# Performance work log

Measured on AMD Instinct MI355X. Metric: run time of the kernel, lower is better.

## Reference

```python
import jax, jax.numpy as jnp
import numpy as np

VOCAB, D, PATCH, ROUNDS = 256, 64, 4, 3
B, T = 32, 8192


def setup_inputs() -> dict:
    key = jax.random.key(0)
    ks = jax.random.split(key, 16)
    s = 0.02
    inp = {
        "x": jax.random.randint(ks[0], (B, T), 0, VOCAB),
        "emb": jax.random.normal(ks[1], (VOCAB, D), jnp.float32) * s,
        # msg_net: Linear(2d->d), GELU, Linear(d->d); weights stored [in, out]
        "w_m1": jax.random.normal(ks[2], (2 * D, D), jnp.float32) * s,
        "b_m1": jnp.zeros((D,), jnp.float32),
        "w_m2": jax.random.normal(ks[3], (D, D), jnp.float32) * s,
        "b_m2": jnp.zeros((D,), jnp.float32),
        # update_net: Linear(2d->d), GELU, Linear(d->d)
        "w_u1": jax.random.normal(ks[4], (2 * D, D), jnp.float32) * s,
        "b_u1": jnp.zeros((D,), jnp.float32),
        "w_u2": jax.random.normal(ks[5], (D, D), jnp.float32) * s,
        "b_u2": jnp.zeros((D,), jnp.float32),
        # LayerNorm(d)
        "ln_g": jnp.ones((D,), jnp.float32),
        "ln_b": jnp.zeros((D,), jnp.float32),
        # readout: Linear(d -> vocab)
        "w_r": jax.random.normal(ks[6], (D, VOCAB), jnp.float32) * s,
        "b_r": jnp.zeros((VOCAB,), jnp.float32),
    }
    return inp


def _mlp(z, w1, b1, w2, b2):
    h = jax.nn.gelu(z @ w1 + b1, approximate=False)  # torch nn.GELU default = exact erf
    return h @ w2 + b2


def _layernorm(h, g, b, eps=1e-5):
    mu = jnp.mean(h, axis=-1, keepdims=True)
    var = jnp.mean((h - mu) ** 2, axis=-1, keepdims=True)
    return (h - mu) / jnp.sqrt(var + eps) * g + b


def reference(x, emb, w_m1, b_m1, w_m2, b_m2, w_u1, b_u1, w_u2, b_u2, ln_g, ln_b, w_r, b_r):
    Bx, Tx = x.shape
    P = PATCH
    N = (Tx + P - 1) // P
    xp = jnp.pad(x, ((0, 0), (0, N * P - Tx)))  # pad token id 0
    h = emb[xp].reshape(Bx, N, P, D).mean(axis=2)  # [B, N, d] patch-node features
    for _ in range(ROUNDS):
        left = jnp.pad(h[:, :-1], ((0, 0), (1, 0), (0, 0)))  # shift-right along N
        msgs = _mlp(jnp.concatenate([h, left], axis=-1), w_m1, b_m1, w_m2, b_m2)
        upd = _mlp(jnp.concatenate([h, msgs], axis=-1), w_u1, b_u1, w_u2, b_u2)
        h = _layernorm(h + upd, ln_g, ln_b)
    tok = jnp.repeat(h, P, axis=1)[:, :Tx]  # broadcast node feat to its P tokens
    return tok @ w_r + b_r  # [B, T, vocab]
```

## Files before the change

kernel.cpp:

```cpp
#include <hip/hip_runtime.h>
#include <hip/hip_bf16.h>
#include <math.h>

#define DD 64
#define NPB 2048
#define RTOT 65536

typedef __bf16 bf16;
typedef bf16 bf16x8 __attribute__((ext_vector_type(8)));
typedef float f32x4 __attribute__((ext_vector_type(4)));
typedef short short4v __attribute__((ext_vector_type(4)));

#define COMPILER_FENCE() asm volatile("" ::: "memory")

__device__ __forceinline__ f32x4 mfma16(bf16x8 a, bf16x8 b, f32x4 c) {
  return __builtin_amdgcn_mfma_f32_16x16x32_bf16(a, b, c, 0, 0, 0);
}

__device__ __forceinline__ float gelu_fast(float x) {
  float u = fabsf(x) * 0.70710678118654752f;
  float t = __builtin_amdgcn_rcpf(fmaf(0.3275911f, u, 1.0f));
  float p = t * fmaf(t, fmaf(t, fmaf(t, fmaf(t, 1.061405429f, -1.453152027f),
                                     1.421413741f), -0.284496736f), 0.254829592f);
  float e = __expf(-u * u);
  float erfa = fmaf(-p, e, 1.0f);
  float s = copysignf(erfa, x);
  return 0.5f * x * (1.0f + s);
}

__device__ __forceinline__ int swz(int col, int row) {
  return col ^ ((row & 7) << 3);
}

__device__ __forceinline__ bf16x8 ld8(const bf16* p) {
  return *reinterpret_cast<const bf16x8*>(p);
}

__global__ void __launch_bounds__(256) k_pe(const int* __restrict__ x,
                                            const float* __restrict__ emb,
                                            const float* __restrict__ wm1,
                                            const float* __restrict__ wm2,
                                            const float* __restrict__ wu1,
                                            const float* __restrict__ wu2,
                                            const float* __restrict__ wr,
                                            bf16* __restrict__ Wsc,
                                            bf16* __restrict__ h) {
  const int b = blockIdx.x;
  if (b < 160) {
    int gid = b * 256 + threadIdx.x;
    if (gid < 8192) {
      int n = gid >> 7, k = gid & 127;
      Wsc[gid] = (bf16)wm1[k * 64 + n];
    } else if (gid < 16384) {
      int j = gid - 8192, n = j >> 7, k = j & 127;
      Wsc[gid] = (bf16)wu1[k * 64 + n];
    } else if (gid < 20480) {
      int j = gid - 16384, n = j >> 6, k = j & 63;
      Wsc[gid] = (bf16)wm2[k * 64 + n];
    } else if (gid < 24576) {
      int j = gid - 20480, n = j >> 6, k = j & 63;
      Wsc[gid] = (bf16)wu2[k * 64 + n];
    } else {
      int j = gid - 24576, v = j >> 6, k = j & 63;
      Wsc[gid] = (bf16)wr[k * 256 + v];
    }
  } else {
    int gid = (b - 160) * 256 + threadIdx.x;
    int row = gid >> 4, d0 = (gid & 15) * 4;
    const int* xp = x + row * 4;
    f32x4 s = {0.f, 0.f, 0.f, 0.f};
#pragma unroll
    for (int p = 0; p < 4; ++p)
      s += *reinterpret_cast<const f32x4*>(emb + xp[p] * DD + d0);
    short4v o;
#pragma unroll
    for (int j = 0; j < 4; ++j)
      o[j] = (short)__builtin_bit_cast(unsigned short, (bf16)(s[j] * 0.25f));
    *reinterpret_cast<short4v*>(h + row * DD + d0) = o;
  }
}

__global__ void __launch_bounds__(256) k_r(const bf16* __restrict__ hin,
                                           bf16* __restrict__ hout,
                                           const bf16* __restrict__ Wsc,
                                           const float* __restrict__ bm1,
                                           const float* __restrict__ bm2,
                                           const float* __restrict__ bu1,
                                           const float* __restrict__ bu2,
                                           const float* __restrict__ lng,
                                           const float* __restrict__ lnb) {
  __shared__ bf16 W1[2][64 * 128];
  __shared__ bf16 Ms[64 * 64];
  __shared__ bf16 Hs[64 * 64];

  const int tid = threadIdx.x;
  const int lane = tid & 63;
  const int wv = tid >> 6;
  const int l15 = lane & 15;
  const int lhi = lane >> 4;

  for (int i = tid; i < 2048; i += 256) {
    int buf = i >> 10, idx = i & 1023;
    int n = idx >> 4, g = (idx & 15) * 8;
    *reinterpret_cast<bf16x8*>(&W1[buf][n * 128 + swz(g, n)]) =
        ld8(Wsc + buf * 8192 + n * 128 + g);
  }
  bf16x8 fm2[4][2], fu2[4][2];
#pragma unroll
  for (int ct = 0; ct < 4; ++ct)
#pragma unroll
    for (int kt = 0; kt < 2; ++kt) {
      int off = (ct * 16 + l15) * 64 + kt * 32 + lhi * 8;
      fm2[ct][kt] = ld8(Wsc + 16384 + off);
      fu2[ct][kt] = ld8(Wsc + 20480 + off);
    }
  float bm1v[4], bm2v[4], bu1v[4], bu2v[4], lngv[4], lnbv[4];
#pragma unroll
  for (int ct = 0; ct < 4; ++ct) {
    int c = ct * 16 + l15;
    bm1v[ct] = bm1[c]; bm2v[ct] = bm2[c];
    bu1v[ct] = bu1[c]; bu2v[ct] = bu2[c];
    lngv[ct] = lng[c]; lnbv[ct] = lnb[c];
  }
  __syncthreads();

  const int lrow = wv * 16 + l15;
  const int sxr = (lrow & 7) << 3;
  const int sxw = (l15 & 7) << 3;
  const f32x4 fz = {0.f, 0.f, 0.f, 0.f};

  for (int tt = 0; tt < 2; ++tt) {
    const int rowbase = (blockIdx.x * 2 + tt) * 64;
    const int grow = rowbase + lrow;
    const bf16* hrow = hin + (size_t)grow * DD;

    bf16x8 ah0 = ld8(hrow + lhi * 8);
    bf16x8 ah1 = ld8(hrow + 32 + lhi * 8);
    bf16x8 al0, al1;
#pragma unroll
    for (int j = 0; j < 8; ++j) { al0[j] = (bf16)0.f; al1[j] = (bf16)0.f; }
    if ((grow & (NPB - 1)) != 0) {
      al0 = ld8(hrow - DD + lhi * 8);
      al1 = ld8(hrow - DD + 32 + lhi * 8);
    }

    f32x4 acc[4];
#pragma unroll
    for (int ct = 0; ct < 4; ++ct) acc[ct] = fz;
#pragma unroll
    for (int ct = 0; ct < 4; ++ct) {
      const bf16* wb = &W1[0][(ct * 16 + l15) * 128];
      acc[ct] = mfma16(ah0, ld8(wb + ((lhi * 8) ^ sxw)), acc[ct]);
      acc[ct] = mfma16(ah1, ld8(wb + ((32 + lhi * 8) ^ sxw)), acc[ct]);
      acc[ct] = mfma16(al0, ld8(wb + ((64 + lhi * 8) ^ sxw)), acc[ct]);
      acc[ct] = mfma16(al1, ld8(wb + ((96 + lhi * 8) ^ sxw)), acc[ct]);
    }
#pragma unroll
    for (int ct = 0; ct < 4; ++ct)
#pragma unroll
      for (int r = 0; r < 4; ++r) {
        float g = gelu_fast(acc[ct][r] + bm1v[ct]);
        int row = wv * 16 + lhi * 4 + r;
        Hs[row * 64 + swz(ct * 16 + l15, row)] = (bf16)g;
      }
    COMPILER_FENCE();
#pragma unroll
    for (int ct = 0; ct < 4; ++ct) acc[ct] = fz;
    {
      bf16x8 g0 = ld8(&Hs[lrow * 64 + ((lhi * 8) ^ sxr)]);
      bf16x8 g1 = ld8(&Hs[lrow * 64 + ((32 + lhi * 8) ^ sxr)]);
#pragma unroll
      for (int ct = 0; ct < 4; ++ct) {
        acc[ct] = mfma16(g0, fm2[ct][0], acc[ct]);
        acc[ct] = mfma16(g1, fm2[ct][1], acc[ct]);
      }
    }
#pragma unroll
    for (int ct = 0; ct < 4; ++ct)
#pragma unroll
      for (int r = 0; r < 4; ++r) {
        int row = wv * 16 + lhi * 4 + r;
        Ms[row * 64 + swz(ct * 16 + l15, row)] = (bf16)(acc[ct][r] + bm2v[ct]);
      }
    COMPILER_FENCE();
#pragma unroll
    for (int ct = 0; ct < 4; ++ct) acc[ct] = fz;
    {
      bf16x8 m0 = ld8(&Ms[lrow * 64 + ((lhi * 8) ^ sxr)]);
      bf16x8 m1 = ld8(&Ms[lrow * 64 + ((32 + lhi * 8) ^ sxr)]);
#pragma unroll
      for (int ct = 0; ct < 4; ++ct) {
        const bf16* wb = &W1[1][(ct * 16 + l15) * 128];
        acc[ct] = mfma16(ah0, ld8(wb + ((lhi * 8) ^ sxw)), acc[ct]);
        acc[ct] = mfma16(ah1, ld8(wb + ((32 + lhi * 8) ^ sxw)), acc[ct]);
        acc[ct] = mfma16(m0, ld8(wb + ((64 + lhi * 8) ^ sxw)), acc[ct]);
        acc[ct] = mfma16(m1, ld8(wb + ((96 + lhi * 8) ^ sxw)), acc[ct]);
      }
    }
    COMPILER_FENCE();
#pragma unroll
    for (int ct = 0; ct < 4; ++ct)
#pragma unroll
      for (int r = 0; r < 4; ++r) {
        float g = gelu_fast(acc[ct][r] + bu1v[ct]);
        int row = wv * 16 + lhi * 4 + r;
        Hs[row * 64 + swz(ct * 16 + l15, row)] = (bf16)g;
      }
    COMPILER_FENCE();
#pragma unroll
    for (int ct = 0; ct < 4; ++ct) acc[ct] = fz;
    {
      bf16x8 u0 = ld8(&Hs[lrow * 64 + ((lhi * 8) ^ sxr)]);
      bf16x8 u1 = ld8(&Hs[lrow * 64 + ((32 + lhi * 8) ^ sxr)]);
#pragma unroll
      for (int ct = 0; ct < 4; ++ct) {
        acc[ct] = mfma16(u0, fu2[ct][0], acc[ct]);
        acc[ct] = mfma16(u1, fu2[ct][1], acc[ct]);
      }
    }
    float xv[4][4];
#pragma unroll
    for (int ct = 0; ct < 4; ++ct)
#pragma unroll
      for (int r = 0; r < 4; ++r) {
        int row = rowbase + wv * 16 + lhi * 4 + r;
        xv[ct][r] = acc[ct][r] + bu2v[ct] + (float)hin[(size_t)row * DD + ct * 16 + l15];
      }
    float s1[4], s2[4];
#pragma unroll
    for (int r = 0; r < 4; ++r) {
      s1[r] = 0.f; s2[r] = 0.f;
#pragma unroll
      for (int ct = 0; ct < 4; ++ct) { s1[r] += xv[ct][r]; s2[r] += xv[ct][r] * xv[ct][r]; }
    }
#pragma unroll
    for (int off = 1; off < 16; off <<= 1)
#pragma unroll
      for (int r = 0; r < 4; ++r) {
        s1[r] += __shfl_xor(s1[r], off);
        s2[r] += __shfl_xor(s2[r], off);
      }
#pragma unroll
    for (int r = 0; r < 4; ++r) {
      float mu = s1[r] * 0.015625f;
      float var = s2[r] * 0.015625f - mu * mu;
      float rstd = rsqrtf(var + 1e-5f);
      int row = rowbase + wv * 16 + lhi * 4 + r;
#pragma unroll
      for (int ct = 0; ct < 4; ++ct)
        hout[(size_t)row * DD + ct * 16 + l15] =
            (bf16)((xv[ct][r] - mu) * rstd * lngv[ct] + lnbv[ct]);
    }
  }
}

__global__ void __launch_bounds__(256) k_r3r(const bf16* __restrict__ hin,
                                             const bf16* __restrict__ Wsc,
                                             const float* __restrict__ bm1,
                                             const float* __restrict__ bm2,
                                             const float* __restrict__ bu1,
                                             const float* __restrict__ bu2,
                                             const float* __restrict__ lng,
                                             const float* __restrict__ lnb,
                                             const float* __restrict__ br,
                                             float* __restrict__ out) {
  __shared__ bf16 W1[2][64 * 128];
  __shared__ bf16 Ms[64 * 64];
  __shared__ bf16 Hs[64 * 64];
  __shared__ bf16 Wt[256 * 64];

  const int tid = threadIdx.x;
  const int lane = tid & 63;
  const int wv = tid >> 6;
  const int l15 = lane & 15;
  const int lhi = lane >> 4;

  for (int i = tid; i < 2048; i += 256) {
    int buf = i >> 10, idx = i & 1023;
    int n = idx >> 4, g = (idx & 15) * 8;
    *reinterpret_cast<bf16x8*>(&W1[buf][n * 128 + swz(g, n)]) =
        ld8(Wsc + buf * 8192 + n * 128 + g);
  }
  {
    const bf16* wrt = Wsc + 24576;
    for (int i = tid; i < 2048; i += 256) {
      int v = i >> 3, g = (i & 7) * 8;
      *reinterpret_cast<bf16x8*>(&Wt[v * 64 + swz(g, v)]) = ld8(wrt + v * 64 + g);
    }
  }
  bf16x8 fm2[4][2], fu2[4][2];
#pragma unroll
  for (int ct = 0; ct < 4; ++ct)
#pragma unroll
    for (int kt = 0; kt < 2; ++kt) {
      int off = (ct * 16 + l15) * 64 + kt * 32 + lhi * 8;
      fm2[ct][kt] = ld8(Wsc + 16384 + off);
      fu2[ct][kt] = ld8(Wsc + 20480 + off);
    }
  float bm1v[4], bm2v[4], bu1v[4], bu2v[4], lngv[4], lnbv[4];
#pragma unroll
  for (int ct = 0; ct < 4; ++ct) {
    int c = ct * 16 + l15;
    bm1v[ct] = bm1[c]; bm2v[ct] = bm2[c];
    bu1v[ct] = bu1[c]; bu2v[ct] = bu2[c];
    lngv[ct] = lng[c]; lnbv[ct] = lnb[c];
  }
  f32x4 brv[16];
#pragma unroll
  for (int vt = 0; vt < 16; ++vt)
    brv[vt] = *reinterpret_cast<const f32x4*>(br + vt * 16 + lhi * 4);
  __syncthreads();

  const int lrow = wv * 16 + l15;
  const int sxr = (lrow & 7) << 3;
  const int sxw = (l15 & 7) << 3;
  const int sxv = (l15 & 7) << 3;
  const f32x4 fz = {0.f, 0.f, 0.f, 0.f};

  bf16x8 pah0, pah1, pal0, pal1;
  float pres[4][4];

#pragma unroll
  for (int tt = 0; tt < 2; ++tt) {
    const int rowbase = (blockIdx.x * 2 + tt) * 64;
    const int grow = rowbase + lrow;
    const bf16* hrow = hin + (size_t)grow * DD;

    bf16x8 ah0, ah1, al0, al1;
    if (tt == 0) {
      ah0 = ld8(hrow + lhi * 8);
      ah1 = ld8(hrow + 32 + lhi * 8);
#pragma unroll
      for (int j = 0; j < 8; ++j) { al0[j] = (bf16)0.f; al1[j] = (bf16)0.f; }
      if ((grow & (NPB - 1)) != 0) {
        al0 = ld8(hrow - DD + lhi * 8);
        al1 = ld8(hrow - DD + 32 + lhi * 8);
      }
    } else {
      ah0 = pah0; ah1 = pah1; al0 = pal0; al1 = pal1;
    }

    f32x4 acc[4];
#pragma unroll
    for (int ct = 0; ct < 4; ++ct) acc[ct] = fz;
#pragma unroll
    for (int ct = 0; ct < 4; ++ct) {
      const bf16* wb = &W1[0][(ct * 16 + l15) * 128];
      acc[ct] = mfma16(ah0, ld8(wb + ((lhi * 8) ^ sxw)), acc[ct]);
      acc[ct] = mfma16(ah1, ld8(wb + ((32 + lhi * 8) ^ sxw)), acc[ct]);
      acc[ct] = mfma16(al0, ld8(wb + ((64 + lhi * 8) ^ sxw)), acc[ct]);
      acc[ct] = mfma16(al1, ld8(wb + ((96 + lhi * 8) ^ sxw)), acc[ct]);
    }
#pragma unroll
    for (int ct = 0; ct < 4; ++ct)
#pragma unroll
      for (int r = 0; r < 4; ++r) {
        float g = gelu_fast(acc[ct][r] + bm1v[ct]);
        int row = wv * 16 + lhi * 4 + r;
        Hs[row * 64 + swz(ct * 16 + l15, row)] = (bf16)g;
      }
    COMPILER_FENCE();
#pragma unroll
    for (int ct = 0; ct < 4; ++ct) acc[ct] = fz;
    {
      bf16x8 g0 = ld8(&Hs[lrow * 64 + ((lhi * 8) ^ sxr)]);
      bf16x8 g1 = ld8(&Hs[lrow * 64 + ((32 + lhi * 8) ^ sxr)]);
#pragma unroll
      for (int ct = 0; ct < 4; ++ct) {
        acc[ct] = mfma16(g0, fm2[ct][0], acc[ct]);
        acc[ct] = mfma16(g1, fm2[ct][1], acc[ct]);
      }
    }
#pragma unroll
    for (int ct = 0; ct < 4; ++ct)
#pragma unroll
      for (int r = 0; r < 4; ++r) {
        int row = wv * 16 + lhi * 4 + r;
        Ms[row * 64 + swz(ct * 16 + l15, row)] = (bf16)(acc[ct][r] + bm2v[ct]);
      }
    COMPILER_FENCE();
#pragma unroll
    for (int ct = 0; ct < 4; ++ct) acc[ct] = fz;
    {
      bf16x8 m0 = ld8(&Ms[lrow * 64 + ((lhi * 8) ^ sxr)]);
      bf16x8 m1 = ld8(&Ms[lrow * 64 + ((32 + lhi * 8) ^ sxr)]);
#pragma unroll
      for (int ct = 0; ct < 4; ++ct) {
        const bf16* wb = &W1[1][(ct * 16 + l15) * 128];
        acc[ct] = mfma16(ah0, ld8(wb + ((lhi * 8) ^ sxw)), acc[ct]);
        acc[ct] = mfma16(ah1, ld8(wb + ((32 + lhi * 8) ^ sxw)), acc[ct]);
        acc[ct] = mfma16(m0, ld8(wb + ((64 + lhi * 8) ^ sxw)), acc[ct]);
        acc[ct] = mfma16(m1, ld8(wb + ((96 + lhi * 8) ^ sxw)), acc[ct]);
      }
    }
    COMPILER_FENCE();
#pragma unroll
    for (int ct = 0; ct < 4; ++ct)
#pragma unroll
      for (int r = 0; r < 4; ++r) {
        float g = gelu_fast(acc[ct][r] + bu1v[ct]);
        int row = wv * 16 + lhi * 4 + r;
        Hs[row * 64 + swz(ct * 16 + l15, row)] = (bf16)g;
      }
    COMPILER_FENCE();
#pragma unroll
    for (int ct = 0; ct < 4; ++ct) acc[ct] = fz;
    {
      bf16x8 u0 = ld8(&Hs[lrow * 64 + ((lhi * 8) ^ sxr)]);
      bf16x8 u1 = ld8(&Hs[lrow * 64 + ((32 + lhi * 8) ^ sxr)]);
#pragma unroll
      for (int ct = 0; ct < 4; ++ct) {
        acc[ct] = mfma16(u0, fu2[ct][0], acc[ct]);
        acc[ct] = mfma16(u1, fu2[ct][1], acc[ct]);
      }
    }
    float xv[4][4];
#pragma unroll
    for (int ct = 0; ct < 4; ++ct)
#pragma unroll
      for (int r = 0; r < 4; ++r) {
        if (tt == 0) {
          int row = rowbase + wv * 16 + lhi * 4 + r;
          xv[ct][r] = acc[ct][r] + bu2v[ct] + (float)hin[(size_t)row * DD + ct * 16 + l15];
        } else {
          xv[ct][r] = acc[ct][r] + bu2v[ct] + pres[ct][r];
        }
      }
    float s1[4], s2[4];
#pragma unroll
    for (int r = 0; r < 4; ++r) {
      s1[r] = 0.f; s2[r] = 0.f;
#pragma unroll
      for (int ct = 0; ct < 4; ++ct) { s1[r] += xv[ct][r]; s2[r] += xv[ct][r] * xv[ct][r]; }
    }
#pragma unroll
    for (int off = 1; off < 16; off <<= 1)
#pragma unroll
      for (int r = 0; r < 4; ++r) {
        s1[r] += __shfl_xor(s1[r], off);
        s2[r] += __shfl_xor(s2[r], off);
      }
#pragma unroll
    for (int r = 0; r < 4; ++r) {
      float mu = s1[r] * 0.015625f;
      float var = s2[r] * 0.015625f - mu * mu;
      float rstd = rsqrtf(var + 1e-5f);
      int row = wv * 16 + lhi * 4 + r;
#pragma unroll
      for (int ct = 0; ct < 4; ++ct)
        Ms[row * 64 + swz(ct * 16 + l15, row)] =
            (bf16)((xv[ct][r] - mu) * rstd * lngv[ct] + lnbv[ct]);
    }
    COMPILER_FENCE();

    if (tt == 0) {
      const int grow1 = grow + 64;
      const bf16* hrow1 = hin + (size_t)grow1 * DD;
      pah0 = ld8(hrow1 + lhi * 8);
      pah1 = ld8(hrow1 + 32 + lhi * 8);
#pragma unroll
      for (int j = 0; j < 8; ++j) { pal0[j] = (bf16)0.f; pal1[j] = (bf16)0.f; }
      if ((grow1 & (NPB - 1)) != 0) {
        pal0 = ld8(hrow1 - DD + lhi * 8);
        pal1 = ld8(hrow1 - DD + 32 + lhi * 8);
      }
#pragma unroll
      for (int ct = 0; ct < 4; ++ct)
#pragma unroll
        for (int r = 0; r < 4; ++r) {
          int row = rowbase + 64 + wv * 16 + lhi * 4 + r;
          pres[ct][r] = (float)hin[(size_t)row * DD + ct * 16 + l15];
        }
    }

    {
      bf16x8 b0 = ld8(&Ms[lrow * 64 + ((lhi * 8) ^ sxr)]);
      bf16x8 b1 = ld8(&Ms[lrow * 64 + ((32 + lhi * 8) ^ sxr)]);
      const int node = rowbase + lrow;
      float* ob = out + (size_t)node * 1024 + lhi * 4;
#pragma unroll
      for (int vt = 0; vt < 16; ++vt) {
        const bf16* wb = &Wt[(vt * 16 + l15) * 64];
        bf16x8 a0 = ld8(wb + ((lhi * 8) ^ sxv));
        bf16x8 a1 = ld8(wb + ((32 + lhi * 8) ^ sxv));
        f32x4 a = mfma16(a0, b0, brv[vt]);
        a = mfma16(a1, b1, a);
        float* p = ob + vt * 16;
#pragma unroll
        for (int rep = 0; rep < 4; ++rep)
          *reinterpret_cast<f32x4*>(p + rep * 256) = a;
      }
    }
    COMPILER_FENCE();
  }
}

extern "C" void kernel_launch(void* const* d_in, const int* in_sizes, int n_in,
                              void* d_out, int out_size, void* d_ws, size_t ws_size,
                              hipStream_t stream) {
  const int*   x   = (const int*)d_in[0];
  const float* emb = (const float*)d_in[1];
  const float* wm1 = (const float*)d_in[2];
  const float* bm1 = (const float*)d_in[3];
  const float* wm2 = (const float*)d_in[4];
  const float* bm2 = (const float*)d_in[5];
  const float* wu1 = (const float*)d_in[6];
  const float* bu1 = (const float*)d_in[7];
  const float* wu2 = (const float*)d_in[8];
  const float* bu2 = (const float*)d_in[9];
  const float* lng = (const float*)d_in[10];
  const float* lnb = (const float*)d_in[11];
  const float* wr  = (const float*)d_in[12];
  const float* br  = (const float*)d_in[13];
  float* out = (float*)d_out;

  char* ws = (char*)d_ws;
  bf16* hA  = (bf16*)ws;
  bf16* hB  = (bf16*)(ws + (size_t)RTOT * DD * 2);
  bf16* Wsc = (bf16*)(ws + (size_t)RTOT * DD * 4);

  hipLaunchKernelGGL(k_pe, dim3(4256), dim3(256), 0, stream,
                     x, emb, wm1, wm2, wu1, wu2, wr, Wsc, hA);
  hipLaunchKernelGGL(k_r, dim3(512), dim3(256), 0, stream,
                     hA, hB, Wsc, bm1, bm2, bu1, bu2, lng, lnb);
  hipLaunchKernelGGL(k_r, dim3(512), dim3(256), 0, stream,
                     hB, hA, Wsc, bm1, bm2, bu1, bu2, lng, lnb);
  hipLaunchKernelGGL(k_r3r, dim3(512), dim3(256), 0, stream,
                     hA, Wsc, bm1, bm2, bu1, bu2, lng, lnb, br, out);
}
```

Measured before the change: 112.1 us.

## Fuse patch embedding into first message-passing round kernel

The patch-embedding gather and mean is moved out of the weight-prep kernel and into a new first-round kernel that builds each 64-row tile (plus one halo row) directly in shared memory. This avoids writing the initial h to global memory and reading it back in round one. The cost is a recomputed halo row per tile and embedding gathers now serialized ahead of the MFMA work in the round kernel. Weight conversion runs as its own small kernel.

```diff
diff --git a/kernel.cpp b/kernel.cpp
--- a/kernel.cpp
+++ b/kernel.cpp
@@ -36,47 +36,225 @@
   return *reinterpret_cast<const bf16x8*>(p);
 }
 
-__global__ void __launch_bounds__(256) k_pe(const int* __restrict__ x,
-                                            const float* __restrict__ emb,
-                                            const float* __restrict__ wm1,
-                                            const float* __restrict__ wm2,
-                                            const float* __restrict__ wu1,
-                                            const float* __restrict__ wu2,
-                                            const float* __restrict__ wr,
-                                            bf16* __restrict__ Wsc,
-                                            bf16* __restrict__ h) {
-  const int b = blockIdx.x;
-  if (b < 160) {
-    int gid = b * 256 + threadIdx.x;
-    if (gid < 8192) {
-      int n = gid >> 7, k = gid & 127;
-      Wsc[gid] = (bf16)wm1[k * 64 + n];
-    } else if (gid < 16384) {
-      int j = gid - 8192, n = j >> 7, k = j & 127;
-      Wsc[gid] = (bf16)wu1[k * 64 + n];
-    } else if (gid < 20480) {
-      int j = gid - 16384, n = j >> 6, k = j & 63;
-      Wsc[gid] = (bf16)wm2[k * 64 + n];
-    } else if (gid < 24576) {
-      int j = gid - 20480, n = j >> 6, k = j & 63;
-      Wsc[gid] = (bf16)wu2[k * 64 + n];
-    } else {
-      int j = gid - 24576, v = j >> 6, k = j & 63;
-      Wsc[gid] = (bf16)wr[k * 256 + v];
-    }
+__global__ void __launch_bounds__(256) k_prep(const float* __restrict__ wm1,
+                                              const float* __restrict__ wm2,
+                                              const float* __restrict__ wu1,
+                                              const float* __restrict__ wu2,
+                                              const float* __restrict__ wr,
+                                              bf16* __restrict__ Wsc) {
+  int gid = blockIdx.x * 256 + threadIdx.x;
+  if (gid < 8192) {
+    int n = gid >> 7, k = gid & 127;
+    Wsc[gid] = (bf16)wm1[k * 64 + n];
+  } else if (gid < 16384) {
+    int j = gid - 8192, n = j >> 7, k = j & 127;
+    Wsc[gid] = (bf16)wu1[k * 64 + n];
+  } else if (gid < 20480) {
+    int j = gid - 16384, n = j >> 6, k = j & 63;
+    Wsc[gid] = (bf16)wm2[k * 64 + n];
+  } else if (gid < 24576) {
+    int j = gid - 20480, n = j >> 6, k = j & 63;
+    Wsc[gid] = (bf16)wu2[k * 64 + n];
   } else {
-    int gid = (b - 160) * 256 + threadIdx.x;
-    int row = gid >> 4, d0 = (gid & 15) * 4;
-    const int* xp = x + row * 4;
-    f32x4 s = {0.f, 0.f, 0.f, 0.f};
-#pragma unroll
-    for (int p = 0; p < 4; ++p)
-      s += *reinterpret_cast<const f32x4*>(emb + xp[p] * DD + d0);
-    short4v o;
-#pragma unroll
-    for (int j = 0; j < 4; ++j)
-      o[j] = (short)__builtin_bit_cast(unsigned short, (bf16)(s[j] * 0.25f));
-    *reinterpret_cast<short4v*>(h + row * DD + d0) = o;
+    int j = gid - 24576, v = j >> 6, k = j & 63;
+    Wsc[gid] = (bf16)wr[k * 256 + v];
+  }
+}
+
+__global__ void __launch_bounds__(256) k_er1(const int* __restrict__ x,
+                                             const float* __restrict__ emb,
+                                             const bf16* __restrict__ Wsc,
+                                             const float* __restrict__ bm1,
+                                             const float* __restrict__ bm2,
+                                             const float* __restrict__ bu1,
+                                             const float* __restrict__ bu2,
+                                             const float* __restrict__ lng,
+                                             const float* __restrict__ lnb,
+                                             bf16* __restrict__ hout) {
+  __shared__ bf16 W1[2][64 * 128];
+  __shared__ bf16 Ms[64 * 64];
+  __shared__ bf16 Hs[64 * 64];
+  __shared__ bf16 Hb[65 * 64];
+
+  const int tid = threadIdx.x;
+  const int lane = tid & 63;
+  const int wv = tid >> 6;
+  const int l15 = lane & 15;
+  const int lhi = lane >> 4;
+
+  for (int i = tid; i < 2048; i += 256) {
+    int buf = i >> 10, idx = i & 1023;
+    int n = idx >> 4, g = (idx & 15) * 8;
+    *reinterpret_cast<bf16x8*>(&W1[buf][n * 128 + swz(g, n)]) =
+        ld8(Wsc + buf * 8192 + n * 128 + g);
+  }
+  bf16x8 fm2[4][2], fu2[4][2];
+#pragma unroll
+  for (int ct = 0; ct < 4; ++ct)
+#pragma unroll
+    for (int kt = 0; kt < 2; ++kt) {
+      int off = (ct * 16 + l15) * 64 + kt * 32 + lhi * 8;
+      fm2[ct][kt] = ld8(Wsc + 16384 + off);
+      fu2[ct][kt] = ld8(Wsc + 20480 + off);
+    }
+  float bm1v[4], bm2v[4], bu1v[4], bu2v[4], lngv[4], lnbv[4];
+#pragma unroll
+  for (int ct = 0; ct < 4; ++ct) {
+    int c = ct * 16 + l15;
+    bm1v[ct] = bm1[c]; bm2v[ct] = bm2[c];
+    bu1v[ct] = bu1[c]; bu2v[ct] = bu2[c];
+    lngv[ct] = lng[c]; lnbv[ct] = lnb[c];
+  }
+
+  const int lrow = wv * 16 + l15;
+  const int sxr = (lrow & 7) << 3;
+  const int sxw = (l15 & 7) << 3;
+  const f32x4 fz = {0.f, 0.f, 0.f, 0.f};
+
+  for (int tt = 0; tt < 2; ++tt) {
+    const int rowbase = (blockIdx.x * 2 + tt) * 64;
+
+    for (int i = tid; i < 65 * 16; i += 256) {
+      int r16 = i >> 4, d0 = (i & 15) * 4;
+      int ge = rowbase - 1 + r16;
+      int gx = ge < 0 ? 0 : ge;
+      const int* xp = x + gx * 4;
+      f32x4 s = {0.f, 0.f, 0.f, 0.f};
+#pragma unroll
+      for (int p = 0; p < 4; ++p)
+        s += *reinterpret_cast<const f32x4*>(emb + xp[p] * DD + d0);
+      short4v o;
+#pragma unroll
+      for (int j = 0; j < 4; ++j)
+        o[j] = (short)__builtin_bit_cast(unsigned short, (bf16)(s[j] * 0.25f));
+      *reinterpret_cast<short4v*>(&Hb[r16 * 64 + swz(d0, r16)]) = o;
+    }
+    __syncthreads();
+
+    const int grow = rowbase + lrow;
+    const int a = 1 + lrow;
+    const int sxa = (a & 7) << 3;
+
+    bf16x8 ah0 = ld8(&Hb[a * 64 + ((lhi * 8) ^ sxa)]);
+    bf16x8 ah1 = ld8(&Hb[a * 64 + ((32 + lhi * 8) ^ sxa)]);
+    bf16x8 al0, al1;
+#pragma unroll
+    for (int j = 0; j < 8; ++j) { al0[j] = (bf16)0.f; al1[j] = (bf16)0.f; }
+    if ((grow & (NPB - 1)) != 0) {
+      int p = a - 1, sxp = (p & 7) << 3;
+      al0 = ld8(&Hb[p * 64 + ((lhi * 8) ^ sxp)]);
+      al1 = ld8(&Hb[p * 64 + ((32 + lhi * 8) ^ sxp)]);
+    }
+
+    f32x4 acc[4];
+#pragma unroll
+    for (int ct = 0; ct < 4; ++ct) acc[ct] = fz;
+#pragma unroll
+    for (int ct = 0; ct < 4; ++ct) {
+      const bf16* wb = &W1[0][(ct * 16 + l15) * 128];
+      acc[ct] = mfma16(ah0, ld8(wb + ((lhi * 8) ^ sxw)), acc[ct]);
+      acc[ct] = mfma16(ah1, ld8(wb + ((32 + lhi * 8) ^ sxw)), acc[ct]);
+      acc[ct] = mfma16(al0, ld8(wb + ((64 + lhi * 8) ^ sxw)), acc[ct]);
+      acc[ct] = mfma16(al1, ld8(wb + ((96 + lhi * 8) ^ sxw)), acc[ct]);
+    }
+#pragma unroll
+    for (int ct = 0; ct < 4; ++ct)
+#pragma unroll
+      for (int r = 0; r < 4; ++r) {
+        float g = gelu_fast(acc[ct][r] + bm1v[ct]);
+        int row = wv * 16 + lhi * 4 + r;
+        Hs[row * 64 + swz(ct * 16 + l15, row)] = (bf16)g;
+      }
+    COMPILER_FENCE();
+#pragma unroll
+    for (int ct = 0; ct < 4; ++ct) acc[ct] = fz;
+    {
+      bf16x8 g0 = ld8(&Hs[lrow * 64 + ((lhi * 8) ^ sxr)]);
+      bf16x8 g1 = ld8(&Hs[lrow * 64 + ((32 + lhi * 8) ^ sxr)]);
+#pragma unroll
+      for (int ct = 0; ct < 4; ++ct) {
+        acc[ct] = mfma16(g0, fm2[ct][0], acc[ct]);
+        acc[ct] = mfma16(g1, fm2[ct][1], acc[ct]);
+      }
+    }
+#pragma unroll
+    for (int ct = 0; ct < 4; ++ct)
+#pragma unroll
+      for (int r = 0; r < 4; ++r) {
+        int row = wv * 16 + lhi * 4 + r;
+        Ms[row * 64 + swz(ct * 16 + l15, row)] = (bf16)(acc[ct][r] + bm2v[ct]);
+      }
+    COMPILER_FENCE();
+#pragma unroll
+    for (int ct = 0; ct < 4; ++ct) acc[ct] = fz;
+    {
+      bf16x8 m0 = ld8(&Ms[lrow * 64 + ((lhi * 8) ^ sxr)]);
+      bf16x8 m1 = ld8(&Ms[lrow * 64 + ((32 + lhi * 8) ^ sxr)]);
+#pragma unroll
+      for (int ct = 0; ct < 4; ++ct) {
+        const bf16* wb = &W1[1][(ct * 16 + l15) * 128];
+        acc[ct] = mfma16(ah0, ld8(wb + ((lhi * 8) ^ sxw)), acc[ct]);
+        acc[ct] = mfma16(ah1, ld8(wb + ((32 + lhi * 8) ^ sxw)), acc[ct]);
+        acc[ct] = mfma16(m0, ld8(wb + ((64 + lhi * 8) ^ sxw)), acc[ct]);
+        acc[ct] = mfma16(m1, ld8(wb + ((96 + lhi * 8) ^ sxw)), acc[ct]);
+      }
+    }
+    COMPILER_FENCE();
+#pragma unroll
+    for (int ct = 0; ct < 4; ++ct)
+#pragma unroll
+      for (int r = 0; r < 4; ++r) {
+        float g = gelu_fast(acc[ct][r] + bu1v[ct]);
+        int row = wv * 16 + lhi * 4 + r;
+        Hs[row * 64 + swz(ct * 16 + l15, row)] = (bf16)g;
+      }
+    COMPILER_FENCE();
+#pragma unroll
+    for (int ct = 0; ct < 4; ++ct) acc[ct] = fz;
+    {
+      bf16x8 u0 = ld8(&Hs[lrow * 64 + ((lhi * 8) ^ sxr)]);
+      bf16x8 u1 = ld8(&Hs[lrow * 64 + ((32 + lhi * 8) ^ sxr)]);
+#pragma unroll
+      for (int ct = 0; ct < 4; ++ct) {
+        acc[ct] = mfma16(u0, fu2[ct][0], acc[ct]);
+        acc[ct] = mfma16(u1, fu2[ct][1], acc[ct]);
+      }
+    }
+    float xv[4][4];
+#pragma unroll
+    for (int ct = 0; ct < 4; ++ct)
+#pragma unroll
+      for (int r = 0; r < 4; ++r) {
+        int b = 1 + wv * 16 + lhi * 4 + r;
+        xv[ct][r] = acc[ct][r] + bu2v[ct] +
+                    (float)Hb[b * 64 + swz(ct * 16 + l15, b)];
+      }
+    float s1[4], s2[4];
+#pragma unroll
+    for (int r = 0; r < 4; ++r) {
+      s1[r] = 0.f; s2[r] = 0.f;
+#pragma unroll
+      for (int ct = 0; ct < 4; ++ct) { s1[r] += xv[ct][r]; s2[r] += xv[ct][r] * xv[ct][r]; }
+    }
+#pragma unroll
+    for (int off = 1; off < 16; off <<= 1)
+#pragma unroll
+      for (int r = 0; r < 4; ++r) {
+        s1[r] += __shfl_xor(s1[r], off);
+        s2[r] += __shfl_xor(s2[r], off);
+      }
+#pragma unroll
+    for (int r = 0; r < 4; ++r) {
+      float mu = s1[r] * 0.015625f;
+      float var = s2[r] * 0.015625f - mu * mu;
+      float rstd = rsqrtf(var + 1e-5f);
+      int row = rowbase + wv * 16 + lhi * 4 + r;
+#pragma unroll
+      for (int ct = 0; ct < 4; ++ct)
+        hout[(size_t)row * DD + ct * 16 + l15] =
+            (bf16)((xv[ct][r] - mu) * rstd * lngv[ct] + lnbv[ct]);
+    }
+    __syncthreads();
   }
 }
 
@@ -519,10 +697,10 @@
   bf16* hB  = (bf16*)(ws + (size_t)RTOT * DD * 2);
   bf16* Wsc = (bf16*)(ws + (size_t)RTOT * DD * 4);
 
-  hipLaunchKernelGGL(k_pe, dim3(4256), dim3(256), 0, stream,
-                     x, emb, wm1, wm2, wu1, wu2, wr, Wsc, hA);
-  hipLaunchKernelGGL(k_r, dim3(512), dim3(256), 0, stream,
-                     hA, hB, Wsc, bm1, bm2, bu1, bu2, lng, lnb);
+  hipLaunchKernelGGL(k_prep, dim3(160), dim3(256), 0, stream,
+                     wm1, wm2, wu1, wu2, wr, Wsc);
+  hipLaunchKernelGGL(k_er1, dim3(512), dim3(256), 0, stream,
+                     x, emb, Wsc, bm1, bm2, bu1, bu2, lng, lnb, hB);
   hipLaunchKernelGGL(k_r, dim3(512), dim3(256), 0, stream,
                      hB, hA, Wsc, bm1, bm2, bu1, bu2, lng, lnb);
   hipLaunchKernelGGL(k_r3r, dim3(512), dim3(256), 0, stream,
```

New measurement: 113.9 us. No clear change (+1.6%).
